# Kernel optimization log

Hardware: AMD Instinct MI355X
Metric: run time of the kernel (lower is better)

The kernel has to match this reference:

```python
import jax, jax.numpy as jnp
import numpy as np

KSIZE = 20      # gaussian smoothing kernel size
SIGMA = 2.0     # gaussianSmoothWidth
STRIDE = 4      # strideLen
KLEN = 14       # kernelLen
LN_EPS = 1e-5


def _gauss_smooth(x):
    # x: [B, T, D]; depthwise conv1d along time, padding='same' (torch: left 9, right 10)
    D = x.shape[-1]
    i = jnp.arange(KSIZE, dtype=x.dtype)
    g = jnp.exp(-0.5 * ((i - (KSIZE - 1) / 2.0) / SIGMA) ** 2)
    g = g / jnp.sum(g)
    k = jnp.tile(g[None, None, :], (D, 1, 1))  # [D, 1, KSIZE]
    y = jax.lax.conv_general_dilated(
        jnp.swapaxes(x, 1, 2), k,
        window_strides=(1,), padding=[(9, 10)],
        feature_group_count=D,
        dimension_numbers=('NCW', 'OIW', 'NCW'))
    return jnp.swapaxes(y, 1, 2)


def _qrnn_layer(x, W, b):
    # SpeechBrain QuasiRNNLayer (output_gate=True, unidirectional, zoneout=0)
    # x: [B, T, F]; W: [3H, 2F]; b: [3H]
    xprev = jnp.concatenate([jnp.zeros_like(x[:, :1]), x[:, :-1]], axis=1)
    y = jnp.einsum('btf,gf->btg', jnp.concatenate([x, xprev], axis=-1), W) + b
    z, f, o = jnp.split(y, 3, axis=-1)
    z = jnp.tanh(z)
    f = jax.nn.sigmoid(f)
    fz = f * z
    # recurrence: c_t = f_t*z_t + (1-f_t)*c_{t-1}, c_0-input = 0
    def step(c, ins):
        f_t, fz_t = ins
        c = fz_t + (1.0 - f_t) * c
        return c, c
    c0 = jnp.zeros((f.shape[0], f.shape[2]), f.dtype)
    _, cs = jax.lax.scan(step, c0, (jnp.swapaxes(f, 0, 1), jnp.swapaxes(fz, 0, 1)))
    c = jnp.swapaxes(cs, 0, 1)  # [B, T, H]
    return jax.nn.sigmoid(o) * c


def reference(neuralInput, dayWeights, dayBias, w0, b0, w_rest, b_rest,
              ln_gamma, ln_beta, w_out, b_out, dayIdx):
    x = _gauss_smooth(neuralInput)                    # [B, T, D]
    Wd = dayWeights[dayIdx]                           # [B, D, D]
    bd = dayBias[dayIdx]                              # [B, 1, D]
    x = jnp.einsum('btd,bdk->btk', x, Wd) + bd
    x = x / (1.0 + jnp.abs(x))                        # Softsign
    B, T, D = x.shape
    Tp = (T - KLEN) // STRIDE + 1
    idx = jnp.arange(Tp)[:, None] * STRIDE + jnp.arange(KLEN)[None, :]
    win = x[:, idx, :]                                # [B, Tp, K, D]
    # torch Unfold ordering: channel-major -> feature index = d*KLEN + k
    strided = jnp.transpose(win, (0, 1, 3, 2)).reshape(B, Tp, D * KLEN)
    h = _qrnn_layer(strided, w0, b0)
    for i in range(w_rest.shape[0]):
        h = _qrnn_layer(h, w_rest[i], b_rest[i])
    mu = jnp.mean(h, axis=-1, keepdims=True)
    var = jnp.mean(jnp.square(h - mu), axis=-1, keepdims=True)
    hn = (h - mu) * jax.lax.rsqrt(var + LN_EPS) * ln_gamma + ln_beta
    return jnp.einsum('bth,ch->btc', hn, w_out) + b_out


def setup_inputs() -> dict:
    key = jax.random.key(0)
    ks = jax.random.split(key, 10)
    B, T, D, H, L, NDAYS, C = 32, 2000, 256, 512, 3, 24, 41
    F0 = D * KLEN  # 3584
    inp = {}
    inp['neuralInput'] = jax.random.normal(ks[0], (B, T, D), jnp.float32)
    inp['dayIdx'] = jax.random.randint(ks[1], (B,), 0, NDAYS, jnp.int64 if jax.config.jax_enable_x64 else jnp.int32)
    eye = jnp.eye(D, dtype=jnp.float32)
    inp['dayWeights'] = eye[None] + 0.02 * jax.random.normal(ks[2], (NDAYS, D, D), jnp.float32)
    inp['dayBias'] = jnp.zeros((NDAYS, 1, D), jnp.float32)
    inp['w0'] = jax.random.normal(ks[3], (3 * H, 2 * F0), jnp.float32) / np.sqrt(2 * F0)
    inp['b0'] = jnp.zeros((3 * H,), jnp.float32)
    inp['w_rest'] = jax.random.normal(ks[4], (L - 1, 3 * H, 2 * H), jnp.float32) / np.sqrt(2 * H)
    inp['b_rest'] = jnp.zeros((L - 1, 3 * H), jnp.float32)
    inp['ln_gamma'] = jnp.ones((H,), jnp.float32)
    inp['ln_beta'] = jnp.zeros((H,), jnp.float32)
    inp['w_out'] = jax.random.normal(ks[5], (C, H), jnp.float32) / np.sqrt(H)
    inp['b_out'] = jnp.zeros((C,), jnp.float32)
    return inp
```

## Files before the change

kernel.cpp:

```cpp
#include <hip/hip_runtime.h>
#include <hip/hip_bf16.h>

typedef __hip_bfloat16 bf16;
typedef __attribute__((ext_vector_type(8))) short bf16x8;
typedef __attribute__((ext_vector_type(4))) float f32x4;

#define GT 16
__global__ __launch_bounds__(256) void gauss_kernel(const float* __restrict__ X,
                                                    bf16* __restrict__ Y, int T) {
  int b = blockIdx.y, t0 = blockIdx.x * GT;
  int tid = threadIdx.x;
  __shared__ float xs[GT + 19][256];
  const float* xb = X + (long)b * T * 256;
  for (int r = 0; r < GT + 19; ++r) {
    int tt = t0 + r - 9;
    xs[r][tid] = (tt >= 0 && tt < T) ? xb[(long)tt * 256 + tid] : 0.f;
  }
  __syncthreads();
  float g[20];
  float norm = 0.f;
#pragma unroll
  for (int j = 0; j < 20; ++j) {
    float u = (j - 9.5f) * 0.5f;
    g[j] = expf(-0.5f * u * u);
    norm += g[j];
  }
  float rn = 1.f / norm;
  for (int i = 0; i < GT; ++i) {
    int t = t0 + i;
    if (t >= T) break;
    float acc = 0.f;
#pragma unroll
    for (int j = 0; j < 20; ++j) acc += g[j] * xs[i + j][tid];
    Y[((long)b * T + t) * 256 + tid] = (bf16)(acc * rn);
  }
}

__global__ __launch_bounds__(256) void transpose_day(const float* __restrict__ W,
                                                     bf16* __restrict__ Wt) {
  __shared__ float tile[64][65];
  int d0 = blockIdx.x * 64, g0 = blockIdx.y * 64, day = blockIdx.z;
  const float* Wd = W + (long)day * 65536;
  int tx = threadIdx.x & 63, ty = threadIdx.x >> 6;
  for (int i = 0; i < 16; ++i) {
    int d = ty + i * 4;
    tile[d][tx] = Wd[(long)(d0 + d) * 256 + g0 + tx];
  }
  __syncthreads();
  bf16* out = Wt + (long)day * 65536;
  for (int i = 0; i < 16; ++i) {
    int g = ty + i * 4;
    out[(long)(g0 + g) * 256 + d0 + tx] = (bf16)tile[tx][g];
  }
}

__global__ void buildV_kernel(const float* __restrict__ w0, bf16* __restrict__ V) {
  long idx = (long)blockIdx.x * 256 + threadIdx.x;
  const long total = 18L * 1536 * 256;
  if (idx >= total) return;
  int u = (int)(idx / (1536 * 256));
  int r = (int)(idx % (1536 * 256));
  int g = r >> 8, d = r & 255;
  float v = 0.f;
  if (u < 14) v += w0[(long)g * 7168 + 3584 + d * 14 + u];
  if (u >= 4) v += w0[(long)g * 7168 + d * 14 + (u - 4)];
  V[idx] = (bf16)v;
}

__global__ void conv_wrest(const float* __restrict__ in, bf16* __restrict__ out, long n) {
  long i = (long)blockIdx.x * 256 + threadIdx.x;
  if (i >= n) return;
  long g = i >> 10;
  int k = (int)(i & 1023);
  out[i] = (bf16)in[(g << 10) | (long)(k ^ 512)];
}

__global__ void conv_w0half(const float* __restrict__ in, bf16* __restrict__ out) {
  long i = (long)blockIdx.x * 256 + threadIdx.x;
  const long n = 1536L * 3584;
  if (i >= n) return;
  long g = i / 3584;
  int j = (int)(i - g * 3584);
  out[i] = (bf16)in[g * 7168 + j];
}

__global__ void zero_pads(bf16* __restrict__ h1s, bf16* __restrict__ h2s) {
  int i = blockIdx.x * 256 + threadIdx.x;
  if (i >= 16384) return;
  int b = i >> 9, k = i & 511;
  h1s[(long)b * 498 * 512 + k] = (bf16)0.f;
  h2s[(long)b * 498 * 512 + k] = (bf16)0.f;
}

__global__ __launch_bounds__(256) void mfma_gemm(
    const bf16* __restrict__ A, const bf16* __restrict__ W,
    const float* __restrict__ bias, float* __restrict__ Yf,
    bf16* __restrict__ Yb, const int* __restrict__ dayIdx,
    long astride, int Ta, int D, int rstride, int Tm, int N, int tstride,
    int ntaps, int tap_off0, long wsg, long wst, long dayWStride,
    int dayBStride, int epilogue) {
  int b = blockIdx.z;
  int t0 = blockIdx.y * 128, g0 = blockIdx.x * 128;
  const bf16* Ab = A + (long)b * astride;
  long wbase = 0;
  int boff = 0;
  if (dayIdx) {
    int di = dayIdx[b];
    wbase = (long)di * dayWStride;
    boff = di * dayBStride;
  }
  __shared__ __align__(16) bf16 Al[2][128 * 64];
  __shared__ __align__(16) bf16 Wl[2][128 * 64];
  int tid = threadIdx.x;
  int lane = tid & 63;
  int wave = tid >> 6;
  int wm = (wave >> 1) * 64, wn = (wave & 1) * 64;
  int lr = lane & 15, lg = lane >> 4;
  int srow = tid >> 3, su = tid & 7;
  int nch = D >> 6;
  int niter = ntaps * nch;
  f32x4 acc[4][4] = {};
  bf16x8 ra[4], rw[4];

  auto issue = [&](int it) {
    int tap = it / nch;
    int d0 = (it - tap * nch) << 6;
    int off = tap + tap_off0;
    const bf16* Wtap = W + wbase + (long)tap * wst;
#pragma unroll
    for (int i = 0; i < 4; ++i) {
      int m = srow + i * 32;
      int t = t0 + m;
      int time = t * tstride + off;
      bf16x8 v = {};
      if (t < Tm && time >= 0 && time < Ta)
        v = *reinterpret_cast<const bf16x8*>(Ab + (long)time * rstride + d0 + su * 8);
      ra[i] = v;
      rw[i] = *reinterpret_cast<const bf16x8*>(Wtap + (long)(g0 + m) * wsg + d0 + su * 8);
    }
  };
  auto write_lds = [&](int bufi) {
#pragma unroll
    for (int i = 0; i < 4; ++i) {
      int m = srow + i * 32;
      *reinterpret_cast<bf16x8*>(&Al[bufi][m * 64 + ((su ^ (m & 7)) << 3)]) = ra[i];
      *reinterpret_cast<bf16x8*>(&Wl[bufi][m * 64 + ((su ^ (m & 7)) << 3)]) = rw[i];
    }
  };

  issue(0);
  write_lds(0);
  __syncthreads();
  int cur = 0;
  for (int it = 0; it < niter; ++it) {
    if (it + 1 < niter) issue(it + 1);
#pragma unroll
    for (int kc = 0; kc < 2; ++kc) {
      int ub = kc * 4 + lg;
      bf16x8 af[4], bw[4];
#pragma unroll
      for (int f = 0; f < 4; ++f) {
        int m = wm + f * 16 + lr;
        af[f] = *reinterpret_cast<const bf16x8*>(&Al[cur][m * 64 + ((ub ^ (m & 7)) << 3)]);
        int g = wn + f * 16 + lr;
        bw[f] = *reinterpret_cast<const bf16x8*>(&Wl[cur][g * 64 + ((ub ^ (g & 7)) << 3)]);
      }
      __builtin_amdgcn_s_setprio(1);
#pragma unroll
      for (int fm = 0; fm < 4; ++fm)
#pragma unroll
        for (int fn = 0; fn < 4; ++fn)
          acc[fm][fn] = __builtin_amdgcn_mfma_f32_16x16x32_bf16(af[fm], bw[fn],
                                                                acc[fm][fn], 0, 0, 0);
      __builtin_amdgcn_s_setprio(0);
    }
    if (it + 1 < niter) write_lds(cur ^ 1);
    __syncthreads();
    cur ^= 1;
  }
#pragma unroll
  for (int fn = 0; fn < 4; ++fn) {
    int gcol = g0 + wn + fn * 16 + lr;
    float bb = bias[boff + gcol];
#pragma unroll
    for (int fm = 0; fm < 4; ++fm) {
#pragma unroll
      for (int r = 0; r < 4; ++r) {
        int t = t0 + wm + fm * 16 + lg * 4 + r;
        if (t >= Tm) continue;
        float v = acc[fm][fn][r] + bb;
        if (epilogue == 1) {
          v = v / (1.f + fabsf(v));
          Yb[((long)b * Tm + t) * N + gcol] = (bf16)v;
        } else {
          Yf[((long)b * Tm + t) * N + gcol] = v;
        }
      }
    }
  }
}

__global__ void build_A0(const bf16* __restrict__ xs, bf16* __restrict__ A0) {
  int idx = blockIdx.x * 256 + threadIdx.x;
  if (idx >= 32 * 3584) return;
  int b = idx / 3584, j = idx % 3584;
  int d = j / 14, u = j % 14;
  A0[idx] = xs[((long)b * 2000 + u) * 256 + d];
}

__global__ __launch_bounds__(256) void t0_gemm(const bf16* __restrict__ A0,
                                               const bf16* __restrict__ W0b,
                                               float* __restrict__ part) {
  int g0 = blockIdx.x * 128;
  int ks = blockIdx.y;
  int k0 = ks * 512;
  __shared__ __align__(16) bf16 Wl[128 * 64];
  __shared__ __align__(16) bf16 Alds[32 * 64];
  int tid = threadIdx.x;
  int lane = tid & 63, wave = tid >> 6;
  int wn = wave * 32;
  int lr = lane & 15, lg = lane >> 4;
  int srow = tid >> 3, su = tid & 7;
  f32x4 acc[2][2] = {};
  for (int c = 0; c < 8; ++c) {
    int d0 = k0 + c * 64;
#pragma unroll
    for (int i = 0; i < 4; ++i) {
      int m = srow + i * 32;
      *reinterpret_cast<bf16x8*>(&Wl[m * 64 + ((su ^ (m & 7)) << 3)]) =
          *reinterpret_cast<const bf16x8*>(W0b + (long)(g0 + m) * 3584 + d0 + su * 8);
    }
    {
      int m = srow;
      *reinterpret_cast<bf16x8*>(&Alds[m * 64 + ((su ^ (m & 7)) << 3)]) =
          *reinterpret_cast<const bf16x8*>(A0 + (long)m * 3584 + d0 + su * 8);
    }
    __syncthreads();
#pragma unroll
    for (int kc = 0; kc < 2; ++kc) {
      int ub = kc * 4 + lg;
      bf16x8 am[2], bw[2];
#pragma unroll
      for (int f = 0; f < 2; ++f) {
        int m = f * 16 + lr;
        am[f] = *reinterpret_cast<const bf16x8*>(&Alds[m * 64 + ((ub ^ (m & 7)) << 3)]);
        int g = wn + f * 16 + lr;
        bw[f] = *reinterpret_cast<const bf16x8*>(&Wl[g * 64 + ((ub ^ (g & 7)) << 3)]);
      }
#pragma unroll
      for (int fm = 0; fm < 2; ++fm)
#pragma unroll
        for (int fn = 0; fn < 2; ++fn)
          acc[fm][fn] = __builtin_amdgcn_mfma_f32_16x16x32_bf16(am[fm], bw[fn],
                                                                acc[fm][fn], 0, 0, 0);
    }
    __syncthreads();
  }
#pragma unroll
  for (int fn = 0; fn < 2; ++fn) {
    int gcol = g0 + wn + fn * 16 + lr;
#pragma unroll
    for (int fm = 0; fm < 2; ++fm)
#pragma unroll
      for (int r = 0; r < 4; ++r) {
        int brow = fm * 16 + lg * 4 + r;
        part[((long)ks * 32 + brow) * 1536 + gcol] = acc[fm][fn][r];
      }
  }
}

__global__ void t0_reduce(const float* __restrict__ part, const float* __restrict__ b0,
                          float* __restrict__ y, int Tp) {
  int idx = blockIdx.x * 256 + threadIdx.x;
  if (idx >= 32 * 1536) return;
  int b = idx / 1536, g = idx % 1536;
  float s = b0[g];
#pragma unroll
  for (int k = 0; k < 7; ++k) s += part[((long)k * 32 + b) * 1536 + g];
  y[(long)b * Tp * 1536 + g] = s;
}

#define NC 8
#define LC 63
__device__ __forceinline__ float fsig(float x) { return 1.f / (1.f + __expf(-x)); }
__device__ __forceinline__ float ftanh(float x) { return 1.f - 2.f / (1.f + __expf(2.f * x)); }

__global__ __launch_bounds__(256) void scan_pass1(const float* __restrict__ Yv,
                                                  float* __restrict__ Afac,
                                                  float* __restrict__ Bfac, int Tp) {
  int idx = blockIdx.x * 256 + threadIdx.x;
  int ci = idx >> 14;
  int chain = idx & 16383;
  int b = chain >> 9, hh = chain & 511;
  const float* yb = Yv + (long)b * Tp * 1536 + hh;
  int t0 = ci * LC, t1 = min(t0 + LC, Tp);
  float A = 1.f, Bv = 0.f;
  for (int t = t0; t < t1; ++t) {
    const float* p = yb + (long)t * 1536;
    float z = p[0], f = p[512];
    float fs = fsig(f);
    Bv = fs * ftanh(z) + (1.f - fs) * Bv;
    A *= (1.f - fs);
  }
  Afac[idx] = A;
  Bfac[idx] = Bv;
}

__global__ void scan_pass2(const float* __restrict__ Afac, const float* __restrict__ Bfac,
                           float* __restrict__ cst) {
  int chain = blockIdx.x * 256 + threadIdx.x;
  float c = 0.f;
#pragma unroll
  for (int ci = 0; ci < NC; ++ci) {
    cst[ci * 16384 + chain] = c;
    c = Afac[ci * 16384 + chain] * c + Bfac[ci * 16384 + chain];
  }
}

__global__ __launch_bounds__(256) void scan_pass3(const float* __restrict__ Yv,
                                                  const float* __restrict__ cst,
                                                  bf16* __restrict__ H, int Tp) {
  int idx = blockIdx.x * 256 + threadIdx.x;
  int ci = idx >> 14;
  int chain = idx & 16383;
  int b = chain >> 9, hh = chain & 511;
  const float* yb = Yv + (long)b * Tp * 1536 + hh;
  bf16* hb = H + ((long)b * 498 + 1) * 512 + hh;
  int t0 = ci * LC, t1 = min(t0 + LC, Tp);
  float c = cst[ci * 16384 + chain];
  for (int t = t0; t < t1; ++t) {
    const float* p = yb + (long)t * 1536;
    float z = p[0], f = p[512], o = p[1024];
    float fs = fsig(f);
    c = fs * ftanh(z) + (1.f - fs) * c;
    hb[(long)t * 512] = (bf16)(fsig(o) * c);
  }
}

__global__ __launch_bounds__(256) void ln_out_kernel(
    const bf16* __restrict__ Hs, const float* __restrict__ gamma,
    const float* __restrict__ beta, const float* __restrict__ Wo,
    const float* __restrict__ bo, float* __restrict__ Out) {
  long bt = blockIdx.x;
  int b = (int)(bt / 497), t = (int)(bt % 497);
  const bf16* hrow = Hs + ((long)b * 498 + 1 + t) * 512;
  int tid = threadIdx.x;
  float v0 = (float)hrow[tid], v1 = (float)hrow[tid + 256];
  float s = v0 + v1, s2 = v0 * v0 + v1 * v1;
#pragma unroll
  for (int d = 32; d; d >>= 1) {
    s += __shfl_down(s, d);
    s2 += __shfl_down(s2, d);
  }
  __shared__ float rs[4], rs2[4];
  int wid = tid >> 6, lane = tid & 63;
  if (lane == 0) {
    rs[wid] = s;
    rs2[wid] = s2;
  }
  __syncthreads();
  float sum = rs[0] + rs[1] + rs[2] + rs[3];
  float sum2 = rs2[0] + rs2[1] + rs2[2] + rs2[3];
  float mu = sum * (1.f / 512.f);
  float var = sum2 * (1.f / 512.f) - mu * mu;
  float rstd = rsqrtf(var + 1e-5f);
  __shared__ float hl[512];
  hl[tid] = (v0 - mu) * rstd * gamma[tid] + beta[tid];
  hl[tid + 256] = (v1 - mu) * rstd * gamma[tid + 256] + beta[tid + 256];
  __syncthreads();
  const float4* hp = reinterpret_cast<const float4*>(&hl[lane * 8]);
  float4 h0v = hp[0], h1v = hp[1];
  for (int c = wid; c < 41; c += 4) {
    const float4* wp = reinterpret_cast<const float4*>(Wo + (long)c * 512 + lane * 8);
    float4 w0v = wp[0], w1v = wp[1];
    float a = w0v.x * h0v.x + w0v.y * h0v.y + w0v.z * h0v.z + w0v.w * h0v.w +
              w1v.x * h1v.x + w1v.y * h1v.y + w1v.z * h1v.z + w1v.w * h1v.w;
#pragma unroll
    for (int d = 32; d; d >>= 1) a += __shfl_down(a, d);
    if (lane == 0) Out[bt * 41 + c] = a + bo[c];
  }
}

extern "C" void kernel_launch(void* const* d_in, const int* in_sizes, int n_in,
                              void* d_out, int out_size, void* d_ws, size_t ws_size,
                              hipStream_t stream) {
  const float* neuralInput = (const float*)d_in[0];
  const int* dayIdx = (const int*)d_in[1];
  const float* dayWeights = (const float*)d_in[2];
  const float* dayBias = (const float*)d_in[3];
  const float* w0 = (const float*)d_in[4];
  const float* b0 = (const float*)d_in[5];
  const float* w_rest = (const float*)d_in[6];
  const float* b_rest = (const float*)d_in[7];
  const float* ln_gamma = (const float*)d_in[8];
  const float* ln_beta = (const float*)d_in[9];
  const float* w_out = (const float*)d_in[10];
  const float* b_out = (const float*)d_in[11];
  float* out = (float*)d_out;

  const int B = 32, T = 2000, Tp = 497;

  char* p = (char*)d_ws;
  float* y = (float*)p;   p += 97714176;
  bf16* xs0b = (bf16*)p;  p += 32768000;
  bf16* xs = (bf16*)p;    p += 32768000;
  bf16* Vb = (bf16*)p;    p += 14155776;
  bf16* dWb = (bf16*)p;   p += 3145728;
  bf16* wrb = (bf16*)p;   p += 6291456;
  bf16* w0b = (bf16*)p;   p += 11010048;
  bf16* A0 = (bf16*)p;    p += 229376;
  float* part = (float*)p; p += 1376256;
  bf16* h1s = (bf16*)p;   p += 16320512;
  bf16* h2s = (bf16*)p;   p += 16320512;
  float* Afac = (float*)p; p += 524288;
  float* Bfac = (float*)p; p += 524288;
  float* cst = (float*)p;  p += 524288;

  hipLaunchKernelGGL(zero_pads, dim3(64), dim3(256), 0, stream, h1s, h2s);
  hipLaunchKernelGGL(gauss_kernel, dim3((T + GT - 1) / GT, B), dim3(256), 0, stream,
                     neuralInput, xs0b, T);
  hipLaunchKernelGGL(transpose_day, dim3(4, 4, 24), dim3(256), 0, stream, dayWeights, dWb);
  hipLaunchKernelGGL(buildV_kernel, dim3((18L * 1536 * 256 + 255) / 256), dim3(256), 0,
                     stream, w0, Vb);
  hipLaunchKernelGGL(conv_wrest, dim3((2L * 1536 * 1024 + 255) / 256), dim3(256), 0,
                     stream, w_rest, wrb, 2L * 1536 * 1024);
  hipLaunchKernelGGL(conv_w0half, dim3((1536L * 3584 + 255) / 256), dim3(256), 0,
                     stream, w0, w0b);
  hipLaunchKernelGGL(mfma_gemm, dim3(2, 16, B), dim3(256), 0, stream, xs0b, dWb,
                     dayBias, (float*)nullptr, xs, dayIdx, (long)T * 256, T, 256, 256,
                     T, 256, 1, 1, 0, 256L, 0L, 65536L, 256, 1);
  hipLaunchKernelGGL(build_A0, dim3((32 * 3584 + 255) / 256), dim3(256), 0, stream, xs, A0);
  hipLaunchKernelGGL(t0_gemm, dim3(12, 7), dim3(256), 0, stream, A0, w0b, part);
  hipLaunchKernelGGL(mfma_gemm, dim3(12, 4, B), dim3(256), 0, stream, xs, Vb, b0, y,
                     (bf16*)nullptr, (const int*)nullptr, (long)T * 256, T, 256, 256,
                     Tp, 1536, 4, 18, -4, 256L, 1536L * 256, 0L, 0, 0);
  hipLaunchKernelGGL(t0_reduce, dim3((32 * 1536 + 255) / 256), dim3(256), 0, stream,
                     part, b0, y, Tp);
  hipLaunchKernelGGL(scan_pass1, dim3(512), dim3(256), 0, stream, y, Afac, Bfac, Tp);
  hipLaunchKernelGGL(scan_pass2, dim3(64), dim3(256), 0, stream, Afac, Bfac, cst);
  hipLaunchKernelGGL(scan_pass3, dim3(512), dim3(256), 0, stream, y, cst, h1s, Tp);
  for (int i = 0; i < 2; ++i) {
    bf16* hin = (i == 0) ? h1s : h2s;
    bf16* hout = (i == 0) ? h2s : h1s;
    hipLaunchKernelGGL(mfma_gemm, dim3(12, 4, B), dim3(256), 0, stream, hin,
                       wrb + (long)i * 1536 * 1024, b_rest + (long)i * 1536, y,
                       (bf16*)nullptr, (const int*)nullptr, 498L * 512, Tp, 1024, 512,
                       Tp, 1536, 1, 1, 0, 1024L, 0L, 0L, 0, 0);
    hipLaunchKernelGGL(scan_pass1, dim3(512), dim3(256), 0, stream, y, Afac, Bfac, Tp);
    hipLaunchKernelGGL(scan_pass2, dim3(64), dim3(256), 0, stream, Afac, Bfac, cst);
    hipLaunchKernelGGL(scan_pass3, dim3(512), dim3(256), 0, stream, y, cst, hout, Tp);
  }
  hipLaunchKernelGGL(ln_out_kernel, dim3(B * Tp), dim3(256), 0, stream, h1s,
                     ln_gamma, ln_beta, w_out, b_out, out);
}
```

Baseline: 944.4 us.

## Add 512-thread GEMM with direct-to-LDS triple-buffered loads and XCD-aware tiling

Adds a new gemm8 kernel for the large layer GEMMs. It uses 256x128 tiles with 8 waves and global_load_lds to copy operands straight into a three-stage LDS ring, with explicit vmcnt waits. Block ids are mapped so that each XCD handles a fixed set of batches, which should improve L2 reuse. Out-of-range time rows read from a zeroed page instead of taking a branch. The old mfma_gemm is reduced to the day-transform path only. The cost is 144KB of dynamic LDS, which limits occupancy to one block per CU, and the rows of the last time tile that go past Tm are loaded from valid memory but their results are discarded.

```diff
diff --git a/kernel.cpp b/kernel.cpp
--- a/kernel.cpp
+++ b/kernel.cpp
@@ -84,31 +84,137 @@
   out[i] = (bf16)in[g * 7168 + j];
 }
 
-__global__ void zero_pads(bf16* __restrict__ h1s, bf16* __restrict__ h2s) {
+__global__ void zero_pads(bf16* __restrict__ h1s, bf16* __restrict__ h2s,
+                          float* __restrict__ zpage) {
   int i = blockIdx.x * 256 + threadIdx.x;
+  if (i < 64) zpage[i] = 0.f;
   if (i >= 16384) return;
   int b = i >> 9, k = i & 511;
   h1s[(long)b * 498 * 512 + k] = (bf16)0.f;
   h2s[(long)b * 498 * 512 + k] = (bf16)0.f;
 }
 
+__global__ __launch_bounds__(512) void gemm8(
+    const bf16* __restrict__ A, const bf16* __restrict__ W,
+    const float* __restrict__ bias, float* __restrict__ Y,
+    const bf16* __restrict__ zpage,
+    long astride, int Ta, int D, int rstride, int Tm, int N, int tstride,
+    int ntaps, int tap_off0, long wsg, long wst) {
+  extern __shared__ char smem[];
+  const int id = blockIdx.x;
+  const int xcd = id & 7, local = id >> 3;
+  const int gi = local >> 4;
+  const int ti = (local >> 2) & 3;
+  const int bi = local & 3;
+  const int b = xcd * 4 + bi;
+  const int g0 = gi * 256, t0 = ti * 128;
+
+  const bf16* Ab = A + (long)b * astride;
+  const int tid = threadIdx.x;
+  const int lane = tid & 63;
+  const int w = tid >> 6;
+  const int wr = w >> 2, wc = w & 3;
+  const int lr = lane & 15, lg = lane >> 4;
+  const int nch = D >> 6;
+  const int ns = ntaps * nch;
+
+  auto stage = [&](int bufi, int s) {
+    int tap = s / nch;
+    int d0 = (s - tap * nch) << 6;
+    const bf16* Wp = W + (long)tap * wst + d0;
+    long base = (long)bufi * 49152;
+#pragma unroll
+    for (int j = 0; j < 6; ++j) {
+      int q = j * 512 + tid;
+      int qw = j * 512 + w * 64;
+      const bf16* src;
+      if (q < 1024) {
+        int row = q >> 3;
+        int u = (q & 7) ^ (row & 7);
+        int time = (t0 + row) * tstride + tap + tap_off0;
+        src = (time >= 0 && time < Ta)
+                  ? Ab + (long)time * rstride + d0 + u * 8
+                  : zpage;
+      } else {
+        int row = (q - 1024) >> 3;
+        int u = (q & 7) ^ (row & 7);
+        src = Wp + (long)(g0 + row) * wsg + u * 8;
+      }
+      auto lp = (__attribute__((address_space(3))) void*)(smem + base + (long)qw * 16);
+      __builtin_amdgcn_global_load_lds(
+          (const __attribute__((address_space(1))) void*)src, lp, 16, 0, 0);
+    }
+  };
+
+  f32x4 acc[4][4] = {};
+
+  stage(0, 0);
+  if (ns > 1) stage(1, 1);
+  for (int s = 0; s < ns; ++s) {
+    int cur = s % 3;
+    if (s + 2 < ns) {
+      stage((s + 2) % 3, s + 2);
+      asm volatile("s_waitcnt vmcnt(12)" ::: "memory");
+    } else if (s + 1 < ns) {
+      asm volatile("s_waitcnt vmcnt(6)" ::: "memory");
+    } else {
+      asm volatile("s_waitcnt vmcnt(0)" ::: "memory");
+    }
+    __builtin_amdgcn_s_barrier();
+    __builtin_amdgcn_sched_barrier(0);
+    const char* bufp = smem + (long)cur * 49152;
+#pragma unroll
+    for (int kc = 0; kc < 2; ++kc) {
+      int ub = kc * 4 + lg;
+      bf16x8 af[4], bw[4];
+#pragma unroll
+      for (int f = 0; f < 4; ++f) {
+        int m = wr * 64 + f * 16 + lr;
+        af[f] = *reinterpret_cast<const bf16x8*>(bufp + m * 128 + ((ub ^ (m & 7)) << 4));
+        int g = wc * 64 + f * 16 + lr;
+        bw[f] = *reinterpret_cast<const bf16x8*>(bufp + 16384 + g * 128 +
+                                                 ((ub ^ (g & 7)) << 4));
+      }
+      __builtin_amdgcn_s_setprio(1);
+#pragma unroll
+      for (int fm = 0; fm < 4; ++fm)
+#pragma unroll
+        for (int fn = 0; fn < 4; ++fn)
+          acc[fm][fn] = __builtin_amdgcn_mfma_f32_16x16x32_bf16(af[fm], bw[fn],
+                                                                acc[fm][fn], 0, 0, 0);
+      __builtin_amdgcn_s_setprio(0);
+    }
+    __builtin_amdgcn_sched_barrier(0);
+    __builtin_amdgcn_s_barrier();
+  }
+
+#pragma unroll
+  for (int fn = 0; fn < 4; ++fn) {
+    int gcol = g0 + wc * 64 + fn * 16 + lr;
+    float bb = bias[gcol];
+#pragma unroll
+    for (int fm = 0; fm < 4; ++fm) {
+#pragma unroll
+      for (int r = 0; r < 4; ++r) {
+        int t = t0 + wr * 64 + fm * 16 + lg * 4 + r;
+        if (t >= Tm) continue;
+        Y[((long)b * Tm + t) * N + gcol] = acc[fm][fn][r] + bb;
+      }
+    }
+  }
+}
+
 __global__ __launch_bounds__(256) void mfma_gemm(
     const bf16* __restrict__ A, const bf16* __restrict__ W,
-    const float* __restrict__ bias, float* __restrict__ Yf,
-    bf16* __restrict__ Yb, const int* __restrict__ dayIdx,
-    long astride, int Ta, int D, int rstride, int Tm, int N, int tstride,
-    int ntaps, int tap_off0, long wsg, long wst, long dayWStride,
-    int dayBStride, int epilogue) {
+    const float* __restrict__ bias, bf16* __restrict__ Yb,
+    const int* __restrict__ dayIdx, long astride, int Ta, int D, int rstride,
+    int Tm, int N, long wsg, long dayWStride, int dayBStride) {
   int b = blockIdx.z;
   int t0 = blockIdx.y * 128, g0 = blockIdx.x * 128;
   const bf16* Ab = A + (long)b * astride;
-  long wbase = 0;
-  int boff = 0;
-  if (dayIdx) {
-    int di = dayIdx[b];
-    wbase = (long)di * dayWStride;
-    boff = di * dayBStride;
-  }
+  int di = dayIdx[b];
+  long wbase = (long)di * dayWStride;
+  int boff = di * dayBStride;
   __shared__ __align__(16) bf16 Al[2][128 * 64];
   __shared__ __align__(16) bf16 Wl[2][128 * 64];
   int tid = threadIdx.x;
@@ -117,26 +223,20 @@
   int wm = (wave >> 1) * 64, wn = (wave & 1) * 64;
   int lr = lane & 15, lg = lane >> 4;
   int srow = tid >> 3, su = tid & 7;
-  int nch = D >> 6;
-  int niter = ntaps * nch;
+  int niter = D >> 6;
   f32x4 acc[4][4] = {};
   bf16x8 ra[4], rw[4];
 
   auto issue = [&](int it) {
-    int tap = it / nch;
-    int d0 = (it - tap * nch) << 6;
-    int off = tap + tap_off0;
-    const bf16* Wtap = W + wbase + (long)tap * wst;
+    int d0 = it << 6;
 #pragma unroll
     for (int i = 0; i < 4; ++i) {
       int m = srow + i * 32;
       int t = t0 + m;
-      int time = t * tstride + off;
       bf16x8 v = {};
-      if (t < Tm && time >= 0 && time < Ta)
-        v = *reinterpret_cast<const bf16x8*>(Ab + (long)time * rstride + d0 + su * 8);
+      if (t < Tm) v = *reinterpret_cast<const bf16x8*>(Ab + (long)t * rstride + d0 + su * 8);
       ra[i] = v;
-      rw[i] = *reinterpret_cast<const bf16x8*>(Wtap + (long)(g0 + m) * wsg + d0 + su * 8);
+      rw[i] = *reinterpret_cast<const bf16x8*>(W + wbase + (long)(g0 + m) * wsg + d0 + su * 8);
     }
   };
   auto write_lds = [&](int bufi) {
@@ -165,14 +265,12 @@
         int g = wn + f * 16 + lr;
         bw[f] = *reinterpret_cast<const bf16x8*>(&Wl[cur][g * 64 + ((ub ^ (g & 7)) << 3)]);
       }
-      __builtin_amdgcn_s_setprio(1);
 #pragma unroll
       for (int fm = 0; fm < 4; ++fm)
 #pragma unroll
         for (int fn = 0; fn < 4; ++fn)
           acc[fm][fn] = __builtin_amdgcn_mfma_f32_16x16x32_bf16(af[fm], bw[fn],
                                                                 acc[fm][fn], 0, 0, 0);
-      __builtin_amdgcn_s_setprio(0);
     }
     if (it + 1 < niter) write_lds(cur ^ 1);
     __syncthreads();
@@ -189,12 +287,8 @@
         int t = t0 + wm + fm * 16 + lg * 4 + r;
         if (t >= Tm) continue;
         float v = acc[fm][fn][r] + bb;
-        if (epilogue == 1) {
-          v = v / (1.f + fabsf(v));
-          Yb[((long)b * Tm + t) * N + gcol] = (bf16)v;
-        } else {
-          Yf[((long)b * Tm + t) * N + gcol] = v;
-        }
+        v = v / (1.f + fabsf(v));
+        Yb[((long)b * Tm + t) * N + gcol] = (bf16)v;
       }
     }
   }
@@ -415,8 +509,11 @@
   float* Afac = (float*)p; p += 524288;
   float* Bfac = (float*)p; p += 524288;
   float* cst = (float*)p;  p += 524288;
-
-  hipLaunchKernelGGL(zero_pads, dim3(64), dim3(256), 0, stream, h1s, h2s);
+  float* zpage = (float*)p; p += 256;
+
+  const int LDS3 = 3 * 49152;
+
+  hipLaunchKernelGGL(zero_pads, dim3(64), dim3(256), 0, stream, h1s, h2s, zpage);
   hipLaunchKernelGGL(gauss_kernel, dim3((T + GT - 1) / GT, B), dim3(256), 0, stream,
                      neuralInput, xs0b, T);
   hipLaunchKernelGGL(transpose_day, dim3(4, 4, 24), dim3(256), 0, stream, dayWeights, dWb);
@@ -427,13 +524,13 @@
   hipLaunchKernelGGL(conv_w0half, dim3((1536L * 3584 + 255) / 256), dim3(256), 0,
                      stream, w0, w0b);
   hipLaunchKernelGGL(mfma_gemm, dim3(2, 16, B), dim3(256), 0, stream, xs0b, dWb,
-                     dayBias, (float*)nullptr, xs, dayIdx, (long)T * 256, T, 256, 256,
-                     T, 256, 1, 1, 0, 256L, 0L, 65536L, 256, 1);
+                     dayBias, xs, dayIdx, (long)T * 256, T, 256, 256, T, 256,
+                     256L, 65536L, 256);
   hipLaunchKernelGGL(build_A0, dim3((32 * 3584 + 255) / 256), dim3(256), 0, stream, xs, A0);
   hipLaunchKernelGGL(t0_gemm, dim3(12, 7), dim3(256), 0, stream, A0, w0b, part);
-  hipLaunchKernelGGL(mfma_gemm, dim3(12, 4, B), dim3(256), 0, stream, xs, Vb, b0, y,
-                     (bf16*)nullptr, (const int*)nullptr, (long)T * 256, T, 256, 256,
-                     Tp, 1536, 4, 18, -4, 256L, 1536L * 256, 0L, 0, 0);
+  hipLaunchKernelGGL(gemm8, dim3(768), dim3(512), LDS3, stream, xs, Vb, b0, y,
+                     (const bf16*)zpage, (long)T * 256, T, 256, 256, Tp, 1536, 4,
+                     18, -4, 256L, 1536L * 256);
   hipLaunchKernelGGL(t0_reduce, dim3((32 * 1536 + 255) / 256), dim3(256), 0, stream,
                      part, b0, y, Tp);
   hipLaunchKernelGGL(scan_pass1, dim3(512), dim3(256), 0, stream, y, Afac, Bfac, Tp);
@@ -442,10 +539,10 @@
   for (int i = 0; i < 2; ++i) {
     bf16* hin = (i == 0) ? h1s : h2s;
     bf16* hout = (i == 0) ? h2s : h1s;
-    hipLaunchKernelGGL(mfma_gemm, dim3(12, 4, B), dim3(256), 0, stream, hin,
+    hipLaunchKernelGGL(gemm8, dim3(768), dim3(512), LDS3, stream, hin,
                        wrb + (long)i * 1536 * 1024, b_rest + (long)i * 1536, y,
-                       (bf16*)nullptr, (const int*)nullptr, 498L * 512, Tp, 1024, 512,
-                       Tp, 1536, 1, 1, 0, 1024L, 0L, 0L, 0, 0);
+                       (const bf16*)zpage, 498L * 512, Tp, 1024, 512, Tp, 1536, 1,
+                       1, 0, 1024L, 0L);
     hipLaunchKernelGGL(scan_pass1, dim3(512), dim3(256), 0, stream, y, Afac, Bfac, Tp);
     hipLaunchKernelGGL(scan_pass2, dim3(64), dim3(256), 0, stream, Afac, Bfac, cst);
     hipLaunchKernelGGL(scan_pass3, dim3(512), dim3(256), 0, stream, y, cst, hout, Tp);
```

Result: faster. 912.5 us (-3.4%).

## Rewrite MFMA GEMM with 256x256 tiles and direct global-to-LDS async loads

Applied to the files above, without the earlier changes.

Replaces the 128x128, 256-thread GEMM with a 512-thread kernel that computes 256x256 output tiles. Operands are streamed straight into double-buffered LDS with global_load_lds, and the overlap is controlled with explicit vmcnt waits and barriers. Out-of-range time rows now read from a zeroed scratch page instead of taking a branch. The aim is more data reuse per tile, no register staging of loads, and a 1D grid with batch-minor ordering that fits in about one wave of blocks. In exchange it needs 128KB of dynamic LDS per block and gives lower occupancy.

```diff
diff --git a/kernel.cpp b/kernel.cpp
--- a/kernel.cpp
+++ b/kernel.cpp
@@ -84,23 +84,31 @@
   out[i] = (bf16)in[g * 7168 + j];
 }
 
-__global__ void zero_pads(bf16* __restrict__ h1s, bf16* __restrict__ h2s) {
+__global__ void zero_pads(bf16* __restrict__ h1s, bf16* __restrict__ h2s,
+                          float* __restrict__ zpage) {
   int i = blockIdx.x * 256 + threadIdx.x;
+  if (i < 64) zpage[i] = 0.f;
   if (i >= 16384) return;
   int b = i >> 9, k = i & 511;
   h1s[(long)b * 498 * 512 + k] = (bf16)0.f;
   h2s[(long)b * 498 * 512 + k] = (bf16)0.f;
 }
 
-__global__ __launch_bounds__(256) void mfma_gemm(
+__global__ __launch_bounds__(512) void gemm8(
     const bf16* __restrict__ A, const bf16* __restrict__ W,
     const float* __restrict__ bias, float* __restrict__ Yf,
     bf16* __restrict__ Yb, const int* __restrict__ dayIdx,
+    const bf16* __restrict__ zpage,
     long astride, int Ta, int D, int rstride, int Tm, int N, int tstride,
     int ntaps, int tap_off0, long wsg, long wst, long dayWStride,
-    int dayBStride, int epilogue) {
-  int b = blockIdx.z;
-  int t0 = blockIdx.y * 128, g0 = blockIdx.x * 128;
+    int dayBStride, int epilogue, int nti) {
+  extern __shared__ char smem[];
+  const int id = blockIdx.x;
+  const int b = id & 31;
+  const int r = id >> 5;
+  const int ti = r % nti, gi = r / nti;
+  const int g0 = gi * 256, t0 = ti * 256;
+
   const bf16* Ab = A + (long)b * astride;
   long wbase = 0;
   int boff = 0;
@@ -109,86 +117,100 @@
     wbase = (long)di * dayWStride;
     boff = di * dayBStride;
   }
-  __shared__ __align__(16) bf16 Al[2][128 * 64];
-  __shared__ __align__(16) bf16 Wl[2][128 * 64];
-  int tid = threadIdx.x;
-  int lane = tid & 63;
-  int wave = tid >> 6;
-  int wm = (wave >> 1) * 64, wn = (wave & 1) * 64;
-  int lr = lane & 15, lg = lane >> 4;
-  int srow = tid >> 3, su = tid & 7;
-  int nch = D >> 6;
-  int niter = ntaps * nch;
-  f32x4 acc[4][4] = {};
-  bf16x8 ra[4], rw[4];
-
-  auto issue = [&](int it) {
-    int tap = it / nch;
-    int d0 = (it - tap * nch) << 6;
-    int off = tap + tap_off0;
-    const bf16* Wtap = W + wbase + (long)tap * wst;
-#pragma unroll
-    for (int i = 0; i < 4; ++i) {
-      int m = srow + i * 32;
-      int t = t0 + m;
-      int time = t * tstride + off;
-      bf16x8 v = {};
-      if (t < Tm && time >= 0 && time < Ta)
-        v = *reinterpret_cast<const bf16x8*>(Ab + (long)time * rstride + d0 + su * 8);
-      ra[i] = v;
-      rw[i] = *reinterpret_cast<const bf16x8*>(Wtap + (long)(g0 + m) * wsg + d0 + su * 8);
+  const int tid = threadIdx.x;
+  const int lane = tid & 63;
+  const int w = tid >> 6;
+  const int wr = w >> 2, wc = w & 3;
+  const int lr = lane & 15, lg = lane >> 4;
+  const int nch = D >> 6;
+  const int ns = ntaps * nch;
+
+  auto stage = [&](int bufi, int s) {
+    int tap = s / nch;
+    int d0 = (s - tap * nch) << 6;
+    const bf16* Wp = W + wbase + (long)tap * wst + d0;
+    long base = (long)bufi * 65536;
+#pragma unroll
+    for (int j = 0; j < 8; ++j) {
+      int q = j * 512 + tid;
+      int qw = j * 512 + w * 64;
+      const bf16* src;
+      if (j < 4) {
+        int row = q >> 3;
+        int u = (q & 7) ^ (row & 7);
+        int time = (t0 + row) * tstride + tap + tap_off0;
+        src = (time >= 0 && time < Ta)
+                  ? Ab + (long)time * rstride + d0 + u * 8
+                  : zpage;
+      } else {
+        int row = (q - 2048) >> 3;
+        int u = (q & 7) ^ (row & 7);
+        src = Wp + (long)(g0 + row) * wsg + u * 8;
+      }
+      auto lp = (__attribute__((address_space(3))) void*)(smem + base + (long)qw * 16);
+      __builtin_amdgcn_global_load_lds(
+          (const __attribute__((address_space(1))) void*)src, lp, 16, 0, 0);
     }
   };
-  auto write_lds = [&](int bufi) {
-#pragma unroll
-    for (int i = 0; i < 4; ++i) {
-      int m = srow + i * 32;
-      *reinterpret_cast<bf16x8*>(&Al[bufi][m * 64 + ((su ^ (m & 7)) << 3)]) = ra[i];
-      *reinterpret_cast<bf16x8*>(&Wl[bufi][m * 64 + ((su ^ (m & 7)) << 3)]) = rw[i];
-    }
-  };
-
-  issue(0);
-  write_lds(0);
-  __syncthreads();
-  int cur = 0;
-  for (int it = 0; it < niter; ++it) {
-    if (it + 1 < niter) issue(it + 1);
+
+  f32x4 acc[8][4] = {};
+
+  stage(0, 0);
+  for (int s = 0; s < ns; ++s) {
+    int cur = s & 1;
+    if (s + 1 < ns) {
+      stage(cur ^ 1, s + 1);
+      asm volatile("s_waitcnt vmcnt(8)" ::: "memory");
+    } else {
+      asm volatile("s_waitcnt vmcnt(0)" ::: "memory");
+    }
+    __builtin_amdgcn_s_barrier();
+    __builtin_amdgcn_sched_barrier(0);
+    const char* bufp = smem + (long)cur * 65536;
 #pragma unroll
     for (int kc = 0; kc < 2; ++kc) {
       int ub = kc * 4 + lg;
-      bf16x8 af[4], bw[4];
+      bf16x8 bw[4];
 #pragma unroll
       for (int f = 0; f < 4; ++f) {
-        int m = wm + f * 16 + lr;
-        af[f] = *reinterpret_cast<const bf16x8*>(&Al[cur][m * 64 + ((ub ^ (m & 7)) << 3)]);
-        int g = wn + f * 16 + lr;
-        bw[f] = *reinterpret_cast<const bf16x8*>(&Wl[cur][g * 64 + ((ub ^ (g & 7)) << 3)]);
-      }
-      __builtin_amdgcn_s_setprio(1);
-#pragma unroll
-      for (int fm = 0; fm < 4; ++fm)
-#pragma unroll
-        for (int fn = 0; fn < 4; ++fn)
-          acc[fm][fn] = __builtin_amdgcn_mfma_f32_16x16x32_bf16(af[fm], bw[fn],
-                                                                acc[fm][fn], 0, 0, 0);
-      __builtin_amdgcn_s_setprio(0);
-    }
-    if (it + 1 < niter) write_lds(cur ^ 1);
-    __syncthreads();
-    cur ^= 1;
-  }
+        int g = wc * 64 + f * 16 + lr;
+        bw[f] = *reinterpret_cast<const bf16x8*>(bufp + 32768 + g * 128 +
+                                                 ((ub ^ (g & 7)) << 4));
+      }
+#pragma unroll
+      for (int fh = 0; fh < 2; ++fh) {
+        bf16x8 af[4];
+#pragma unroll
+        for (int f = 0; f < 4; ++f) {
+          int m = wr * 128 + (fh * 4 + f) * 16 + lr;
+          af[f] = *reinterpret_cast<const bf16x8*>(bufp + m * 128 +
+                                                   ((ub ^ (m & 7)) << 4));
+        }
+        __builtin_amdgcn_s_setprio(1);
+#pragma unroll
+        for (int fm = 0; fm < 4; ++fm)
+#pragma unroll
+          for (int fn = 0; fn < 4; ++fn)
+            acc[fh * 4 + fm][fn] = __builtin_amdgcn_mfma_f32_16x16x32_bf16(
+                af[fm], bw[fn], acc[fh * 4 + fm][fn], 0, 0, 0);
+        __builtin_amdgcn_s_setprio(0);
+      }
+    }
+    __builtin_amdgcn_sched_barrier(0);
+    __builtin_amdgcn_s_barrier();
+  }
+
 #pragma unroll
   for (int fn = 0; fn < 4; ++fn) {
-    int gcol = g0 + wn + fn * 16 + lr;
+    int gcol = g0 + wc * 64 + fn * 16 + lr;
     float bb = bias[boff + gcol];
 #pragma unroll
-    for (int fm = 0; fm < 4; ++fm) {
-#pragma unroll
-      for (int r = 0; r < 4; ++r) {
-        int t = t0 + wm + fm * 16 + lg * 4 + r;
+    for (int fm = 0; fm < 8; ++fm) {
+#pragma unroll
+      for (int rr = 0; rr < 4; ++rr) {
+        int t = t0 + wr * 128 + fm * 16 + lg * 4 + rr;
         if (t >= Tm) continue;
-        float v = acc[fm][fn][r] + bb;
+        float v = acc[fm][fn][rr] + bb;
         if (epilogue == 1) {
           v = v / (1.f + fabsf(v));
           Yb[((long)b * Tm + t) * N + gcol] = (bf16)v;
@@ -415,8 +437,11 @@
   float* Afac = (float*)p; p += 524288;
   float* Bfac = (float*)p; p += 524288;
   float* cst = (float*)p;  p += 524288;
-
-  hipLaunchKernelGGL(zero_pads, dim3(64), dim3(256), 0, stream, h1s, h2s);
+  float* zpage = (float*)p; p += 256;
+
+  const int LDS2 = 2 * 65536;
+
+  hipLaunchKernelGGL(zero_pads, dim3(64), dim3(256), 0, stream, h1s, h2s, zpage);
   hipLaunchKernelGGL(gauss_kernel, dim3((T + GT - 1) / GT, B), dim3(256), 0, stream,
                      neuralInput, xs0b, T);
   hipLaunchKernelGGL(transpose_day, dim3(4, 4, 24), dim3(256), 0, stream, dayWeights, dWb);
@@ -426,14 +451,16 @@
                      stream, w_rest, wrb, 2L * 1536 * 1024);
   hipLaunchKernelGGL(conv_w0half, dim3((1536L * 3584 + 255) / 256), dim3(256), 0,
                      stream, w0, w0b);
-  hipLaunchKernelGGL(mfma_gemm, dim3(2, 16, B), dim3(256), 0, stream, xs0b, dWb,
-                     dayBias, (float*)nullptr, xs, dayIdx, (long)T * 256, T, 256, 256,
-                     T, 256, 1, 1, 0, 256L, 0L, 65536L, 256, 1);
+  hipLaunchKernelGGL(gemm8, dim3(256), dim3(512), LDS2, stream, xs0b, dWb, dayBias,
+                     (float*)nullptr, xs, dayIdx, (const bf16*)zpage,
+                     (long)T * 256, T, 256, 256, T, 256, 1, 1, 0,
+                     256L, 0L, 65536L, 256, 1, 8);
   hipLaunchKernelGGL(build_A0, dim3((32 * 3584 + 255) / 256), dim3(256), 0, stream, xs, A0);
   hipLaunchKernelGGL(t0_gemm, dim3(12, 7), dim3(256), 0, stream, A0, w0b, part);
-  hipLaunchKernelGGL(mfma_gemm, dim3(12, 4, B), dim3(256), 0, stream, xs, Vb, b0, y,
-                     (bf16*)nullptr, (const int*)nullptr, (long)T * 256, T, 256, 256,
-                     Tp, 1536, 4, 18, -4, 256L, 1536L * 256, 0L, 0, 0);
+  hipLaunchKernelGGL(gemm8, dim3(384), dim3(512), LDS2, stream, xs, Vb, b0, y,
+                     (bf16*)nullptr, (const int*)nullptr, (const bf16*)zpage,
+                     (long)T * 256, T, 256, 256, Tp, 1536, 4, 18, -4,
+                     256L, 1536L * 256, 0L, 0, 0, 2);
   hipLaunchKernelGGL(t0_reduce, dim3((32 * 1536 + 255) / 256), dim3(256), 0, stream,
                      part, b0, y, Tp);
   hipLaunchKernelGGL(scan_pass1, dim3(512), dim3(256), 0, stream, y, Afac, Bfac, Tp);
@@ -442,10 +469,11 @@
   for (int i = 0; i < 2; ++i) {
     bf16* hin = (i == 0) ? h1s : h2s;
     bf16* hout = (i == 0) ? h2s : h1s;
-    hipLaunchKernelGGL(mfma_gemm, dim3(12, 4, B), dim3(256), 0, stream, hin,
+    hipLaunchKernelGGL(gemm8, dim3(384), dim3(512), LDS2, stream, hin,
                        wrb + (long)i * 1536 * 1024, b_rest + (long)i * 1536, y,
-                       (bf16*)nullptr, (const int*)nullptr, 498L * 512, Tp, 1024, 512,
-                       Tp, 1536, 1, 1, 0, 1024L, 0L, 0L, 0, 0);
+                       (bf16*)nullptr, (const int*)nullptr, (const bf16*)zpage,
+                       498L * 512, Tp, 1024, 512, Tp, 1536, 1, 1, 0,
+                       1024L, 0L, 0L, 0, 0, 2);
     hipLaunchKernelGGL(scan_pass1, dim3(512), dim3(256), 0, stream, y, Afac, Bfac, Tp);
     hipLaunchKernelGGL(scan_pass2, dim3(64), dim3(256), 0, stream, Afac, Bfac, cst);
     hipLaunchKernelGGL(scan_pass3, dim3(512), dim3(256), 0, stream, y, cst, hout, Tp);
```

Measured after the change: 927.3 us. About the same (-1.8%).
